# Performance work log

Hardware: AMD Instinct MI355X
Metric: run time of the kernel (lower is better)

## Reference

```python
import jax, jax.numpy as jnp
from jax import lax
import numpy as np


def setup_inputs() -> dict:
    key = jax.random.key(0)
    k1, k2 = jax.random.split(key)
    x = jax.random.normal(k1, (8, 256, 64, 64), dtype=jnp.float32)          # [bs, nc, hi, wi]
    templates = jax.random.normal(k2, (8, 8, 256, 7, 7), dtype=jnp.float32)  # [nt, bs, nc, ht, wt]
    return {"x": x, "templates": templates}


def _dw_xcorr_one(x, tmpl):
    # x: [bs, nc, hi, wi]; tmpl: [bs, nc, ht, wt]
    bs, nc, hi, wi = x.shape
    ht, wt = tmpl.shape[-2:]
    pad_h, pad_w = ht // 2, wt // 2
    lhs = x.reshape(1, bs * nc, hi, wi)          # single "image" with bs*nc channels
    rhs = tmpl.reshape(bs * nc, 1, ht, wt)       # one kernel per channel (depthwise)
    out = lax.conv_general_dilated(
        lhs, rhs,
        window_strides=(1, 1),
        padding=[(pad_h, pad_h), (pad_w, pad_w)],
        feature_group_count=bs * nc,
        dimension_numbers=("NCHW", "OIHW", "NCHW"),
    )
    ho, wo = out.shape[-2:]
    return out.reshape(bs, nc, ho, wo)


def reference(x, templates):
    # vmap over the num_templates axis; conv is cross-correlation (matches torch conv2d)
    return jax.vmap(_dw_xcorr_one, in_axes=(None, 0))(x, templates)  # [nt, bs, nc, hi, wi]
```

## Files before the change

kernel.cpp:

```cpp
#include <hip/hip_runtime.h>


#define NT 8
#define BS 8
#define NC 256
#define HW 64
#define PLANE (HW * HW)
#define LROWS 70
#define LSTR  72
#define TPL_STR 52

__global__ __launch_bounds__(256) void dwxcorr_kernel(
    const float* __restrict__ x,
    const float* __restrict__ tm,
    float* __restrict__ out)
{
    __shared__ __align__(16) float xpl[LROWS * LSTR];
    __shared__ __align__(16) float tpl[NT * TPL_STR];

    const int bc  = blockIdx.x;
    const int tid = threadIdx.x;

    for (int i = tid; i < LROWS * LSTR; i += 256) xpl[i] = 0.0f;
    __syncthreads();

    const float* xp = x + bc * PLANE;
    for (int i = tid; i < PLANE / 4; i += 256) {
        float4 v = ((const float4*)xp)[i];
        int row = i >> 4;
        int c4  = (i & 15) << 2;
        *(float4*)&xpl[(row + 3) * LSTR + 4 + c4] = v;
    }

    const float* tb = tm + bc * 49;
    for (int i = tid; i < NT * 49; i += 256) {
        int t = i / 49;
        int k = i - t * 49;
        tpl[t * TPL_STR + k] = tb[t * (NT * NC * 49) + k];
    }
    __syncthreads();

    const int tx = tid & 15, ty = tid >> 4;
    const int col0 = tx << 2, row0 = ty << 2;

    for (int t = 0; t < NT; ++t) {
        float w[TPL_STR];
        const float4* wp = (const float4*)&tpl[t * TPL_STR];
        #pragma unroll
        for (int q = 0; q < TPL_STR / 4; ++q) {
            float4 v = wp[q];
            w[4 * q + 0] = v.x; w[4 * q + 1] = v.y;
            w[4 * q + 2] = v.z; w[4 * q + 3] = v.w;
        }

        float acc[4][4];
        #pragma unroll
        for (int r = 0; r < 4; ++r)
            #pragma unroll
            for (int j = 0; j < 4; ++j) acc[r][j] = 0.0f;

        #pragma unroll
        for (int ir = 0; ir < 10; ++ir) {
            const float* rowp = &xpl[(row0 + ir) * LSTR + col0];
            float xw[12];
            float4 a = *(const float4*)(rowp);
            float4 b = *(const float4*)(rowp + 4);
            float4 c = *(const float4*)(rowp + 8);
            xw[0] = a.x; xw[1]  = a.y; xw[2]  = a.z; xw[3]  = a.w;
            xw[4] = b.x; xw[5]  = b.y; xw[6]  = b.z; xw[7]  = b.w;
            xw[8] = c.x; xw[9]  = c.y; xw[10] = c.z; xw[11] = c.w;

            #pragma unroll
            for (int r = 0; r < 4; ++r) {
                const int ky = ir - r;
                if (ky >= 0 && ky < 7) {
                    #pragma unroll
                    for (int kx = 0; kx < 7; ++kx) {
                        const float tv = w[ky * 7 + kx];
                        #pragma unroll
                        for (int j = 0; j < 4; ++j)
                            acc[r][j] = fmaf(xw[j + kx + 1], tv, acc[r][j]);
                    }
                }
            }
        }

        float* op = out + (size_t)(t * (BS * NC) + bc) * PLANE + row0 * HW + col0;
        #pragma unroll
        for (int r = 0; r < 4; ++r) {
            float4 v = make_float4(acc[r][0], acc[r][1], acc[r][2], acc[r][3]);
            *(float4*)(op + r * HW) = v;
        }
    }
}

extern "C" void kernel_launch(void* const* d_in, const int* in_sizes, int n_in,
                              void* d_out, int out_size, void* d_ws, size_t ws_size,
                              hipStream_t stream) {
    const float* x  = (const float*)d_in[0];
    const float* tm = (const float*)d_in[1];
    float* out = (float*)d_out;
    dwxcorr_kernel<<<BS * NC, 256, 0, stream>>>(x, tm, out);
}
```

Measured before the change: 360.3 us.

## Split templates across waves with 8-row strips and a rolling accumulator window

Each wave now handles 32 rows of the plane for one template per pass, with waves split across template pairs, and each thread computes an 8-row strip. A rolling 7-slot accumulator writes each output row as soon as it is complete. Template weights are read straight from global memory with wave-uniform addresses instead of being staged in shared memory. This raises input-row reuse per thread (14 row loads for 8 outputs instead of 10 for 4) and removes the template staging, at the cost of more live registers and uncached scalar weight loads per pass.

```diff
diff --git a/kernel.cpp b/kernel.cpp
--- a/kernel.cpp
+++ b/kernel.cpp
@@ -8,7 +8,6 @@
 #define PLANE (HW * HW)
 #define LROWS 70
 #define LSTR  72
-#define TPL_STR 52
 
 __global__ __launch_bounds__(256) void dwxcorr_kernel(
     const float* __restrict__ x,
@@ -16,80 +15,76 @@
     float* __restrict__ out)
 {
     __shared__ __align__(16) float xpl[LROWS * LSTR];
-    __shared__ __align__(16) float tpl[NT * TPL_STR];
 
     const int bc  = blockIdx.x;
     const int tid = threadIdx.x;
 
     for (int i = tid; i < LROWS * LSTR; i += 256) xpl[i] = 0.0f;
     __syncthreads();
-
-    const float* xp = x + bc * PLANE;
+    const float* xp = x + (size_t)bc * PLANE;
     for (int i = tid; i < PLANE / 4; i += 256) {
         float4 v = ((const float4*)xp)[i];
         int row = i >> 4;
         int c4  = (i & 15) << 2;
         *(float4*)&xpl[(row + 3) * LSTR + 4 + c4] = v;
     }
-
-    const float* tb = tm + bc * 49;
-    for (int i = tid; i < NT * 49; i += 256) {
-        int t = i / 49;
-        int k = i - t * 49;
-        tpl[t * TPL_STR + k] = tb[t * (NT * NC * 49) + k];
-    }
     __syncthreads();
 
-    const int tx = tid & 15, ty = tid >> 4;
-    const int col0 = tx << 2, row0 = ty << 2;
+    const int lane  = tid & 63;
+    const int wv    = __builtin_amdgcn_readfirstlane(tid >> 6);
+    const int tx    = lane & 15;
+    const int sy    = lane >> 4;
+    const int strip = ((wv & 1) << 2) + sy;
+    const int row0  = strip << 3;
+    const int col0  = tx << 2;
 
-    for (int t = 0; t < NT; ++t) {
-        float w[TPL_STR];
-        const float4* wp = (const float4*)&tpl[t * TPL_STR];
+    #pragma unroll 1
+    for (int p = 0; p < 4; ++p) {
+        const int t = (p << 1) + (wv >> 1);
+
+        const float* wp = tm + ((size_t)t * (BS * NC) + bc) * 49;
+        float w[49];
         #pragma unroll
-        for (int q = 0; q < TPL_STR / 4; ++q) {
-            float4 v = wp[q];
-            w[4 * q + 0] = v.x; w[4 * q + 1] = v.y;
-            w[4 * q + 2] = v.z; w[4 * q + 3] = v.w;
-        }
+        for (int k = 0; k < 49; ++k) w[k] = wp[k];
 
-        float acc[4][4];
+        float4 acc[7];
         #pragma unroll
-        for (int r = 0; r < 4; ++r)
-            #pragma unroll
-            for (int j = 0; j < 4; ++j) acc[r][j] = 0.0f;
+        for (int k = 0; k < 7; ++k) acc[k] = make_float4(0.f, 0.f, 0.f, 0.f);
+
+        float* op = out + ((size_t)t * (BS * NC) + bc) * PLANE + row0 * HW + col0;
 
         #pragma unroll
-        for (int ir = 0; ir < 10; ++ir) {
+        for (int ir = 0; ir < 14; ++ir) {
             const float* rowp = &xpl[(row0 + ir) * LSTR + col0];
-            float xw[12];
             float4 a = *(const float4*)(rowp);
             float4 b = *(const float4*)(rowp + 4);
             float4 c = *(const float4*)(rowp + 8);
-            xw[0] = a.x; xw[1]  = a.y; xw[2]  = a.z; xw[3]  = a.w;
-            xw[4] = b.x; xw[5]  = b.y; xw[6]  = b.z; xw[7]  = b.w;
-            xw[8] = c.x; xw[9]  = c.y; xw[10] = c.z; xw[11] = c.w;
+            const float xw[12] = {a.x, a.y, a.z, a.w,
+                                  b.x, b.y, b.z, b.w,
+                                  c.x, c.y, c.z, c.w};
 
             #pragma unroll
-            for (int r = 0; r < 4; ++r) {
-                const int ky = ir - r;
-                if (ky >= 0 && ky < 7) {
+            for (int ky = 0; ky < 7; ++ky) {
+                const int r = ir - ky;
+                if (r >= 0 && r < 8) {
+                    const int sl = r % 7;
                     #pragma unroll
                     for (int kx = 0; kx < 7; ++kx) {
                         const float tv = w[ky * 7 + kx];
-                        #pragma unroll
-                        for (int j = 0; j < 4; ++j)
-                            acc[r][j] = fmaf(xw[j + kx + 1], tv, acc[r][j]);
+                        acc[sl].x = fmaf(xw[kx + 1], tv, acc[sl].x);
+                        acc[sl].y = fmaf(xw[kx + 2], tv, acc[sl].y);
+                        acc[sl].z = fmaf(xw[kx + 3], tv, acc[sl].z);
+                        acc[sl].w = fmaf(xw[kx + 4], tv, acc[sl].w);
                     }
                 }
             }
-        }
 
-        float* op = out + (size_t)(t * (BS * NC) + bc) * PLANE + row0 * HW + col0;
-        #pragma unroll
-        for (int r = 0; r < 4; ++r) {
-            float4 v = make_float4(acc[r][0], acc[r][1], acc[r][2], acc[r][3]);
-            *(float4*)(op + r * HW) = v;
+            if (ir >= 6) {
+                const int r  = ir - 6;
+                const int sl = r % 7;
+                *(float4*)(op + r * HW) = acc[sl];
+                acc[sl] = make_float4(0.f, 0.f, 0.f, 0.f);
+            }
         }
     }
 }
```

After: 393.2 us. +9.2%, slower.
